# Kernel tuning notes

Hardware: AMD Instinct MI355X
Metric: run time of the kernel (lower is better)

The kernel has to match this reference:

```python
import jax, jax.numpy as jnp
import numpy as np

# Dims per init_kwargs
B, C_IN, H, W = 64, 512, 28, 28
GROWTH, BN_SIZE = 32, 4
C_MID = BN_SIZE * GROWTH  # 128
EPS = 1e-5
NUM_BITS = 8          # activation & weight quantization bits
NUM_CHUNKS = 16       # RangeBN chunking (eladhoffer quantize.py default)


def quantize(x, num_bits):
    """Uniform min/max quantize-dequantize (UniformQuantize forward)."""
    mn = x.min()
    mx = x.max()
    qmax = 2.0 ** num_bits - 1.0
    scale = jnp.maximum((mx - mn) / qmax, 1e-8)
    q = jnp.round((jnp.clip(x, mn, mx) - mn) / scale)
    return q * scale + mn


def conv2d(x, w, pad):
    return jax.lax.conv_general_dilated(
        x, w, window_strides=(1, 1), padding=[(pad, pad), (pad, pad)],
        dimension_numbers=('NCHW', 'OIHW', 'NCHW'))


def batchnorm2d(x, w, b):
    # training-mode BN: batch statistics over (N,H,W), biased variance
    mean = x.mean(axis=(0, 2, 3), keepdims=True)
    var = x.var(axis=(0, 2, 3), keepdims=True)
    xhat = (x - mean) * jax.lax.rsqrt(var + EPS)
    return xhat * w.reshape(1, -1, 1, 1) + b.reshape(1, -1, 1, 1)


def range_bn(x, w, b):
    # Range-based BN (training-mode): per-channel mean, scale from chunked min/max range
    Bx, Cx, Hx, Wx = x.shape
    y = x.transpose(1, 0, 2, 3).reshape(Cx, NUM_CHUNKS, -1)  # [C, chunks, n]
    mean_max = y.max(-1).mean(-1)   # [C]
    mean_min = y.min(-1).mean(-1)   # [C]
    mean = y.reshape(Cx, -1).mean(-1)  # [C]
    n = y.shape[-1]
    scale_fix = (0.5 * 0.35) * (1.0 + (np.pi * np.log(4.0)) ** 0.5) / ((2.0 * np.log(float(n))) ** 0.5)
    scale = 1.0 / ((mean_max - mean_min) * scale_fix + EPS)
    out = (x - mean.reshape(1, Cx, 1, 1)) * scale.reshape(1, Cx, 1, 1)
    qw = quantize(w, NUM_BITS)
    qb = quantize(b, NUM_BITS)
    return out * qw.reshape(1, Cx, 1, 1) + qb.reshape(1, Cx, 1, 1)


def setup_inputs() -> dict:
    key = jax.random.key(0)
    ks = jax.random.split(key, 7)
    x = jax.random.normal(ks[0], (B, C_IN, H, W), dtype=jnp.float32)
    bn1_w = jax.random.uniform(ks[1], (C_IN,), dtype=jnp.float32, minval=0.5, maxval=1.5)
    bn1_b = jax.random.normal(ks[2], (C_IN,), dtype=jnp.float32) * 0.1
    conv1_w = jax.random.normal(ks[3], (C_MID, C_IN, 1, 1), dtype=jnp.float32) * (2.0 / C_IN) ** 0.5
    rbn_w = jax.random.uniform(ks[4], (C_MID,), dtype=jnp.float32, minval=0.5, maxval=1.5)
    rbn_b = jax.random.normal(ks[5], (C_MID,), dtype=jnp.float32) * 0.1
    conv2_w = jax.random.normal(ks[6], (GROWTH, C_MID, 3, 3), dtype=jnp.float32) * (2.0 / (9 * C_MID)) ** 0.5
    return {"x": x, "bn1_w": bn1_w, "bn1_b": bn1_b, "conv1_w": conv1_w,
            "rbn_w": rbn_w, "rbn_b": rbn_b, "conv2_w": conv2_w}


def reference(x, bn1_w, bn1_b, conv1_w, rbn_w, rbn_b, conv2_w):
    # norm1 -> relu1 -> QConv2d(1x1) -> RangeBN -> relu2 -> QConv2d(3x3) -> concat
    h = jax.nn.relu(batchnorm2d(x, bn1_w, bn1_b))
    h = conv2d(quantize(h, NUM_BITS), quantize(conv1_w, NUM_BITS), pad=0)
    h = jax.nn.relu(range_bn(h, rbn_w, rbn_b))
    h = conv2d(quantize(h, NUM_BITS), quantize(conv2_w, NUM_BITS), pad=1)
    # drop_rate = 0 -> dropout is identity
    return jnp.concatenate([x, h], axis=1)
```

## Files before the change

### kernel.cpp

```cpp
#include <hip/hip_runtime.h>
#include <math.h>

static constexpr int BB    = 64;
static constexpr int C_IN  = 512;
static constexpr int C_MID = 128;
static constexpr int C_OUT = 32;
static constexpr int C_TOT = 544;
static constexpr int HW    = 784;

static constexpr size_t H2_OFF    = 0;
static constexpr size_t QW1_OFF   = 6422528;
static constexpr size_t QW2_OFF   = QW1_OFF + 65536;
static constexpr size_t PSTAT_OFF = QW2_OFF + 49152;
static constexpr size_t BNA_OFF   = PSTAT_OFF + 16384;
static constexpr size_t BNB_OFF   = BNA_OFF + 512;
static constexpr size_t CMAX_OFF  = BNB_OFF + 512;
static constexpr size_t CMIN_OFF  = CMAX_OFF + 2048;
static constexpr size_t CSUM_OFF  = CMIN_OFF + 2048;
static constexpr size_t A2_OFF    = CSUM_OFF + 2048;
static constexpr size_t B2_OFF    = A2_OFF + 128;
static constexpr size_t QRW_OFF   = B2_OFF + 128;
static constexpr size_t QRB_OFF   = QRW_OFF + 128;
static constexpr size_t SCAL_OFF  = QRB_OFF + 128;
static constexpr size_t PART_OFF  = SCAL_OFF + 16;
static constexpr size_t RP_OFF    = PART_OFF + 128;
static constexpr size_t PART2_OFF = RP_OFF + 172032;

#define DEVFN __device__ __forceinline__

typedef __bf16 bf16x8 __attribute__((ext_vector_type(8)));
typedef float  f32x4  __attribute__((ext_vector_type(4)));

DEVFN float qact(float v, float mn, float mx, float inv, float sc) {
    v = fminf(fmaxf(v, mn), mx);
    return fmaf(rintf((v - mn) * inv), sc, mn);
}

DEVFN unsigned f2bf(float f) {
    unsigned u = __float_as_uint(f);
    return (u + 0x7fffu + ((u >> 16) & 1u)) >> 16;
}

__global__ __launch_bounds__(256) void k_stats(const float* __restrict__ x,
                                               float* __restrict__ ws) {
    const int c = blockIdx.x, bg = blockIdx.y, tid = threadIdx.x;
    float s = 0.f, s2 = 0.f, mn = INFINITY, mx = -INFINITY;
    if (tid < 224) {
#pragma unroll
        for (int k = 0; k < 7; ++k) {
            const int idx = k * 224 + tid;
            const int b = bg * 8 + idx / 196, j = idx % 196;
            const float4 v = ((const float4*)(x + ((size_t)b * C_IN + c) * HW))[j];
            s  += (v.x + v.y) + (v.z + v.w);
            s2 += v.x * v.x + v.y * v.y + v.z * v.z + v.w * v.w;
            mn = fminf(mn, fminf(fminf(v.x, v.y), fminf(v.z, v.w)));
            mx = fmaxf(mx, fmaxf(fmaxf(v.x, v.y), fmaxf(v.z, v.w)));
        }
    }
    __shared__ float r0[256], r1[256], r2[256], r3[256];
    r0[tid] = s; r1[tid] = s2; r2[tid] = mn; r3[tid] = mx;
    __syncthreads();
    for (int off = 128; off > 0; off >>= 1) {
        if (tid < off) {
            r0[tid] += r0[tid + off];
            r1[tid] += r1[tid + off];
            r2[tid] = fminf(r2[tid], r2[tid + off]);
            r3[tid] = fmaxf(r3[tid], r3[tid + off]);
        }
        __syncthreads();
    }
    if (tid == 0) {
        float* p = ws + PSTAT_OFF + ((size_t)c * 8 + bg) * 4;
        p[0] = r0[0]; p[1] = r1[0]; p[2] = r2[0]; p[3] = r3[0];
    }
}

__global__ __launch_bounds__(256) void k_prep_red(const float* __restrict__ conv1_w,
                                                  const float* __restrict__ conv2_w,
                                                  const float* __restrict__ bn1_w,
                                                  const float* __restrict__ bn1_b,
                                                  float* __restrict__ ws) {
    const int b = blockIdx.x, tid = threadIdx.x;
    __shared__ float ra[256], rb[256];
    float mn = INFINITY, mx = -INFINITY;

    if (b < 32) {
        const float4* src = (const float4*)conv1_w + (size_t)b * 512;
        for (int i = tid; i < 512; i += 256) {
            const float4 v = src[i];
            mn = fminf(mn, fminf(fminf(v.x, v.y), fminf(v.z, v.w)));
            mx = fmaxf(mx, fmaxf(fmaxf(v.x, v.y), fmaxf(v.z, v.w)));
        }
    } else if (b < 40) {
        const float4* src = (const float4*)conv2_w + (size_t)(b - 32) * 1152;
        for (int i = tid; i < 1152; i += 256) {
            const float4 v = src[i];
            mn = fminf(mn, fminf(fminf(v.x, v.y), fminf(v.z, v.w)));
            mx = fmaxf(mx, fmaxf(fmaxf(v.x, v.y), fmaxf(v.z, v.w)));
        }
    } else {
        if (tid < 128) {
            const int c = (b - 40) * 128 + tid;
            const float* p = ws + PSTAT_OFF + (size_t)c * 32;
            float s = 0.f, s2 = 0.f, cmn = INFINITY, cmx = -INFINITY;
            for (int g = 0; g < 8; ++g) {
                s += p[g * 4 + 0]; s2 += p[g * 4 + 1];
                cmn = fminf(cmn, p[g * 4 + 2]); cmx = fmaxf(cmx, p[g * 4 + 3]);
            }
            const float n = 50176.f;
            const float mean = s / n;
            const float var  = s2 / n - mean * mean;
            const float rstd = rsqrtf(var + 1e-5f);
            const float A  = rstd * bn1_w[c];
            const float Bc = bn1_b[c] - mean * A;
            ws[BNA_OFF + c] = A; ws[BNB_OFF + c] = Bc;
            const float v1 = A * cmn + Bc, v2 = A * cmx + Bc;
            mn = fmaxf(0.f, fminf(v1, v2));
            mx = fmaxf(0.f, fmaxf(v1, v2));
        }
    }
    ra[tid] = mn; rb[tid] = mx;
    __syncthreads();
    for (int off = 128; off > 0; off >>= 1) {
        if (tid < off) { ra[tid] = fminf(ra[tid], ra[tid + off]); rb[tid] = fmaxf(rb[tid], rb[tid + off]); }
        __syncthreads();
    }
    if (tid == 0) {
        float* p;
        if (b < 32)       p = ws + PART_OFF + (size_t)b * 2;
        else if (b < 40)  p = ws + PART_OFF + 64 + (size_t)(b - 32) * 2;
        else              p = ws + PART_OFF + 80 + (size_t)(b - 40) * 2;
        p[0] = ra[0]; p[1] = rb[0];
    }
}

__global__ __launch_bounds__(256) void k_prep_fin(const float* __restrict__ rbn_w,
                                                  const float* __restrict__ rbn_b,
                                                  float* __restrict__ ws) {
    const int tid = threadIdx.x;
    __shared__ float ra[256], rb[256];
    __shared__ float s_mn, s_sc;

    ra[tid] = tid < 32 ? ws[PART_OFF + tid * 2] : INFINITY;
    rb[tid] = tid < 32 ? ws[PART_OFF + tid * 2 + 1] : -INFINITY;
    __syncthreads();
    for (int off = 128; off > 0; off >>= 1) {
        if (tid < off) { ra[tid] = fminf(ra[tid], ra[tid + off]); rb[tid] = fmaxf(rb[tid], rb[tid + off]); }
        __syncthreads();
    }
    if (tid == 0) {
        ws[SCAL_OFF + 8] = ra[0];
        ws[SCAL_OFF + 9] = fmaxf((rb[0] - ra[0]) / 255.f, 1e-8f);
    }
    __syncthreads();

    ra[tid] = tid < 8 ? ws[PART_OFF + 64 + tid * 2] : INFINITY;
    rb[tid] = tid < 8 ? ws[PART_OFF + 64 + tid * 2 + 1] : -INFINITY;
    __syncthreads();
    for (int off = 128; off > 0; off >>= 1) {
        if (tid < off) { ra[tid] = fminf(ra[tid], ra[tid + off]); rb[tid] = fmaxf(rb[tid], rb[tid + off]); }
        __syncthreads();
    }
    if (tid == 0) {
        ws[SCAL_OFF + 10] = ra[0];
        ws[SCAL_OFF + 11] = fmaxf((rb[0] - ra[0]) / 255.f, 1e-8f);
    }
    __syncthreads();

    ra[tid] = tid < 4 ? ws[PART_OFF + 80 + tid * 2] : INFINITY;
    rb[tid] = tid < 4 ? ws[PART_OFF + 80 + tid * 2 + 1] : -INFINITY;
    __syncthreads();
    for (int off = 128; off > 0; off >>= 1) {
        if (tid < off) { ra[tid] = fminf(ra[tid], ra[tid + off]); rb[tid] = fmaxf(rb[tid], rb[tid + off]); }
        __syncthreads();
    }
    if (tid == 0) {
        const float mn1 = ra[0], mx1 = rb[0];
        const float sc = fmaxf((mx1 - mn1) / 255.f, 1e-8f);
        ws[SCAL_OFF + 0] = mn1; ws[SCAL_OFF + 1] = sc; ws[SCAL_OFF + 2] = 1.f / sc; ws[SCAL_OFF + 6] = mx1;
    }
    __syncthreads();

    for (int which = 0; which < 2; ++which) {
        const float* src = which ? rbn_b : rbn_w;
        const size_t dst = which ? QRB_OFF : QRW_OFF;
        float v = 0.f;
        ra[tid] = INFINITY; rb[tid] = -INFINITY;
        if (tid < 128) { v = src[tid]; ra[tid] = v; rb[tid] = v; }
        __syncthreads();
        for (int off = 128; off > 0; off >>= 1) {
            if (tid < off) { ra[tid] = fminf(ra[tid], ra[tid + off]); rb[tid] = fmaxf(rb[tid], rb[tid + off]); }
            __syncthreads();
        }
        if (tid == 0) { s_mn = ra[0]; s_sc = fmaxf((rb[0] - ra[0]) / 255.f, 1e-8f); }
        __syncthreads();
        if (tid < 128) ws[dst + tid] = fmaf(rintf((v - s_mn) / s_sc), s_sc, s_mn);
        __syncthreads();
    }
}

__global__ __launch_bounds__(256) void k_prep_quant(const float* __restrict__ conv1_w,
                                                    const float* __restrict__ conv2_w,
                                                    float* __restrict__ ws) {
    const int b = blockIdx.x, tid = threadIdx.x;
    if (b < 32) {
        const float mnw = ws[SCAL_OFF + 8], scw = ws[SCAL_OFF + 9];
        unsigned short* qw = (unsigned short*)(ws + QW1_OFF);
        const int base = b * 2048;
#pragma unroll
        for (int t = 0; t < 8; ++t) {
            const int i = base + t * 256 + tid;
            const int co = i >> 9, k = i & 511;
            const float v = conv1_w[i];
            const float qv = fmaf(rintf((v - mnw) / scw), scw, mnw);
            const int ks = k >> 6, kc = (k >> 3) & 7, klo = k & 7;
            qw[(((size_t)ks * 128 + co) << 6) + (((kc ^ (co & 7)) << 3) | klo)] = (unsigned short)f2bf(qv);
        }
    } else {
        const float mnw = ws[SCAL_OFF + 10], scw = ws[SCAL_OFF + 11];
        unsigned short* qw2 = (unsigned short*)(ws + QW2_OFF);
        const int base = (b - 32) * 4608;
        for (int i2 = tid; i2 < 4608; i2 += 256) {
            const int i = base + i2;
            const int co = i / 1152, r = i % 1152, ci = r / 9, tap = r % 9;
            const float v = conv2_w[i];
            const float qv = fmaf(rintf((v - mnw) / scw), scw, mnw);
            qw2[(size_t)co * 1152 + tap * 128 + ci] = (unsigned short)f2bf(qv);
        }
    }
}

__global__ __launch_bounds__(256, 2) void k_conv1(const float* __restrict__ x,
                                                  float* __restrict__ out,
                                                  float* __restrict__ ws) {
    __shared__ __align__(16) unsigned short wt[128 * 64];
    __shared__ __align__(16) unsigned short ht[112 * 64];
    const int tid = threadIdx.x;
    const int pt = blockIdx.x, b = blockIdx.y;
    const int p0 = pt * 112;
    const float mn1 = ws[SCAL_OFF + 0], sc1 = ws[SCAL_OFF + 1];
    const float inv1 = ws[SCAL_OFF + 2], mx1 = ws[SCAL_OFF + 6];
    const unsigned short* qw1 = (const unsigned short*)(ws + QW1_OFF);
    const float* xb = x + (size_t)b * C_IN * HW;
    float* outb = out + (size_t)b * C_TOT * HW;

    const int o = tid & 7, q = tid >> 3;
    const int wv = tid >> 6, g = (tid >> 4) & 3, r4 = tid & 15;

    f32x4 acc[2][7];
#pragma unroll
    for (int i = 0; i < 2; ++i)
#pragma unroll
        for (int j = 0; j < 7; ++j) acc[i][j] = f32x4{0.f, 0.f, 0.f, 0.f};

    for (int ks = 0; ks < 8; ++ks) {
        const float4* wsrc = (const float4*)(qw1 + (size_t)ks * 8192);
        float4* wdst = (float4*)wt;
#pragma unroll
        for (int i = 0; i < 4; ++i) wdst[tid + i * 256] = wsrc[tid + i * 256];

        if (tid < 224) {
            const int ci0 = ks * 64 + o * 8;
            float vv[8][4];
#pragma unroll
            for (int j = 0; j < 8; ++j) {
                const f32x4 v = *(const f32x4*)(xb + (size_t)(ci0 + j) * HW + p0 + q * 4);
                __builtin_nontemporal_store(v, (f32x4*)(outb + (size_t)(ci0 + j) * HW + p0 + q * 4));
                const float A = ws[BNA_OFF + ci0 + j], Bc = ws[BNB_OFF + ci0 + j];
                vv[j][0] = qact(fmaxf(0.f, fmaf(v.x, A, Bc)), mn1, mx1, inv1, sc1);
                vv[j][1] = qact(fmaxf(0.f, fmaf(v.y, A, Bc)), mn1, mx1, inv1, sc1);
                vv[j][2] = qact(fmaxf(0.f, fmaf(v.z, A, Bc)), mn1, mx1, inv1, sc1);
                vv[j][3] = qact(fmaxf(0.f, fmaf(v.w, A, Bc)), mn1, mx1, inv1, sc1);
            }
#pragma unroll
            for (int r = 0; r < 4; ++r) {
                const int p = q * 4 + r;
                uint4 pk;
                pk.x = f2bf(vv[0][r]) | (f2bf(vv[1][r]) << 16);
                pk.y = f2bf(vv[2][r]) | (f2bf(vv[3][r]) << 16);
                pk.z = f2bf(vv[4][r]) | (f2bf(vv[5][r]) << 16);
                pk.w = f2bf(vv[6][r]) | (f2bf(vv[7][r]) << 16);
                *(uint4*)&ht[p * 64 + ((o ^ (p & 7)) << 3)] = pk;
            }
        }
        __syncthreads();

#pragma unroll
        for (int ksub = 0; ksub < 2; ++ksub) {
            const int kk = ksub * 4 + g;
            bf16x8 af[2], bfr[7];
#pragma unroll
            for (int ct = 0; ct < 2; ++ct) {
                const int co = wv * 32 + ct * 16 + r4;
                af[ct] = *(const bf16x8*)&wt[co * 64 + ((kk ^ (co & 7)) << 3)];
            }
#pragma unroll
            for (int pf = 0; pf < 7; ++pf) {
                const int p = pf * 16 + r4;
                bfr[pf] = *(const bf16x8*)&ht[p * 64 + ((kk ^ (p & 7)) << 3)];
            }
#pragma unroll
            for (int ct = 0; ct < 2; ++ct)
#pragma unroll
                for (int pf = 0; pf < 7; ++pf)
                    acc[ct][pf] = __builtin_amdgcn_mfma_f32_16x16x32_bf16(af[ct], bfr[pf], acc[ct][pf], 0, 0, 0);
        }
        __syncthreads();
    }

    float* hb = ws + H2_OFF + (size_t)b * C_MID * HW;
#pragma unroll
    for (int ct = 0; ct < 2; ++ct) {
        const int co0 = wv * 32 + ct * 16 + g * 4;
#pragma unroll
        for (int pf = 0; pf < 7; ++pf) {
            const int p = p0 + pf * 16 + r4;
#pragma unroll
            for (int r = 0; r < 4; ++r)
                hb[(size_t)(co0 + r) * HW + p] = acc[ct][pf][r];
        }
    }

#pragma unroll
    for (int ct = 0; ct < 2; ++ct)
#pragma unroll
        for (int r = 0; r < 4; ++r) {
            float s = 0.f, mn = INFINITY, mx = -INFINITY;
#pragma unroll
            for (int pf = 0; pf < 7; ++pf) {
                const float v = acc[ct][pf][r];
                s += v; mn = fminf(mn, v); mx = fmaxf(mx, v);
            }
#pragma unroll
            for (int m = 1; m < 16; m <<= 1) {
                s  += __shfl_xor(s, m, 64);
                mn  = fminf(mn, __shfl_xor(mn, m, 64));
                mx  = fmaxf(mx, __shfl_xor(mx, m, 64));
            }
            if (r4 == 0) {
                const int co = wv * 32 + ct * 16 + g * 4 + r;
                float* dst = ws + RP_OFF + (((size_t)co * 64 + b) * 7 + pt) * 3;
                dst[0] = s; dst[1] = mn; dst[2] = mx;
            }
        }
}

__global__ __launch_bounds__(64) void k_rbn_combine(float* __restrict__ ws) {
    const int c = blockIdx.x, t = threadIdx.x;
    const int ch = t >> 2, sub = t & 3;
    const int b = ch * 4 + sub;
    const float* rp = ws + RP_OFF + ((size_t)c * 64 + b) * 21;
    float s = 0.f, mn = INFINITY, mx = -INFINITY;
#pragma unroll
    for (int pt = 0; pt < 7; ++pt) {
        s += rp[pt * 3 + 0];
        mn = fminf(mn, rp[pt * 3 + 1]);
        mx = fmaxf(mx, rp[pt * 3 + 2]);
    }
#pragma unroll
    for (int m = 1; m < 4; m <<= 1) {
        s  += __shfl_xor(s, m, 64);
        mn  = fminf(mn, __shfl_xor(mn, m, 64));
        mx  = fmaxf(mx, __shfl_xor(mx, m, 64));
    }
    float smx = mx, smn = mn, stot = s, gmn = mn, gmx = mx;
#pragma unroll
    for (int m = 4; m < 64; m <<= 1) {
        smx  += __shfl_xor(smx, m, 64);
        smn  += __shfl_xor(smn, m, 64);
        stot += __shfl_xor(stot, m, 64);
        gmn   = fminf(gmn, __shfl_xor(gmn, m, 64));
        gmx   = fmaxf(gmx, __shfl_xor(gmx, m, 64));
    }
    if (t == 0) {
        const float mm = smx * (1.f / 16.f), mnm = smn * (1.f / 16.f);
        const float mean = stot / 50176.f;
        const double PI_D = 3.14159265358979323846;
        const double sfd = 0.175 * (1.0 + sqrt(PI_D * log(4.0))) / sqrt(2.0 * log(3136.0));
        const float scale = 1.f / ((mm - mnm) * (float)sfd + 1e-5f);
        const float A  = scale * ws[QRW_OFF + c];
        const float Bc = ws[QRB_OFF + c] - mean * A;
        ws[A2_OFF + c] = A; ws[B2_OFF + c] = Bc;
        const float v1 = A * gmn + Bc, v2 = A * gmx + Bc;
        ws[PART2_OFF + c * 2 + 0] = fmaxf(0.f, fminf(v1, v2));
        ws[PART2_OFF + c * 2 + 1] = fmaxf(0.f, fmaxf(v1, v2));
    }
}

__global__ __launch_bounds__(64) void k_prep2b(float* __restrict__ ws) {
    const int t = threadIdx.x;
    float lo = fminf(ws[PART2_OFF + t * 2], ws[PART2_OFF + (t + 64) * 2]);
    float hi = fmaxf(ws[PART2_OFF + t * 2 + 1], ws[PART2_OFF + (t + 64) * 2 + 1]);
#pragma unroll
    for (int m = 1; m < 64; m <<= 1) {
        lo = fminf(lo, __shfl_xor(lo, m, 64));
        hi = fmaxf(hi, __shfl_xor(hi, m, 64));
    }
    if (t == 0) {
        const float sc = fmaxf((hi - lo) / 255.f, 1e-8f);
        ws[SCAL_OFF + 3] = lo; ws[SCAL_OFF + 4] = sc; ws[SCAL_OFF + 5] = 1.f / sc; ws[SCAL_OFF + 7] = hi;
    }
}

__global__ __launch_bounds__(128) void k_conv2(float* __restrict__ out, const float* __restrict__ ws) {
    __shared__ __align__(16) unsigned short lact[7 * 30 * 128];
    const int tid = threadIdx.x;
    const int pt = blockIdx.x, b = blockIdx.y;
    const int y0 = pt * 4;
    const float mn3 = ws[SCAL_OFF + 3], sc3 = ws[SCAL_OFF + 4];
    const float inv3 = ws[SCAL_OFF + 5], mx3 = ws[SCAL_OFF + 7];

    {
        const uint4 z = {0u, 0u, 0u, 0u};
        uint4* lp = (uint4*)lact;
        for (int i = tid; i < 3360; i += 128) lp[i] = z;
    }
    __syncthreads();

    const float* h2b = ws + H2_OFF + (size_t)b * C_MID * HW;
    for (int task = tid; task < 672; task += 128) {
        const int oct = task / 42, rem = task % 42, r = rem / 7, xq = rem % 7;
        const int gy = y0 - 1 + r;
        if (gy < 0 || gy > 27) continue;
        float vv[8][4];
#pragma unroll
        for (int j = 0; j < 8; ++j) {
            const int ci = oct * 8 + j;
            const float4 v = *(const float4*)(h2b + (size_t)ci * HW + gy * 28 + xq * 4);
            const float A = ws[A2_OFF + ci], Bc = ws[B2_OFF + ci];
            vv[j][0] = qact(fmaxf(0.f, fmaf(v.x, A, Bc)), mn3, mx3, inv3, sc3);
            vv[j][1] = qact(fmaxf(0.f, fmaf(v.y, A, Bc)), mn3, mx3, inv3, sc3);
            vv[j][2] = qact(fmaxf(0.f, fmaf(v.z, A, Bc)), mn3, mx3, inv3, sc3);
            vv[j][3] = qact(fmaxf(0.f, fmaf(v.w, A, Bc)), mn3, mx3, inv3, sc3);
        }
#pragma unroll
        for (int xi = 0; xi < 4; ++xi) {
            const int col = xq * 4 + xi + 1;
            const int phys = (oct + col) & 15;
            uint4 pk;
            pk.x = f2bf(vv[0][xi]) | (f2bf(vv[1][xi]) << 16);
            pk.y = f2bf(vv[2][xi]) | (f2bf(vv[3][xi]) << 16);
            pk.z = f2bf(vv[4][xi]) | (f2bf(vv[5][xi]) << 16);
            pk.w = f2bf(vv[6][xi]) | (f2bf(vv[7][xi]) << 16);
            *(uint4*)&lact[((r * 30 + col) * 16 + phys) * 8] = pk;
        }
    }
    __syncthreads();

    const int wv = tid >> 6, lane = tid & 63, r4 = lane & 15, g = lane >> 4;
    int py[4], px[4];
#pragma unroll
    for (int i = 0; i < 4; ++i) {
        const int p = (wv * 4 + i) * 16 + r4;
        py[i] = p / 28; px[i] = p % 28;
    }
    f32x4 acc[2][4];
#pragma unroll
    for (int ct = 0; ct < 2; ++ct)
#pragma unroll
        for (int i = 0; i < 4; ++i) acc[ct][i] = f32x4{0.f, 0.f, 0.f, 0.f};

    const unsigned short* qw2 = (const unsigned short*)(ws + QW2_OFF);
    for (int tap = 0; tap < 9; ++tap) {
        const int dy = tap / 3, dx = tap % 3;
        bf16x8 afr[2][4];
#pragma unroll
        for (int ct = 0; ct < 2; ++ct)
#pragma unroll
            for (int c4 = 0; c4 < 4; ++c4) {
                const int co = ct * 16 + r4;
                afr[ct][c4] = *(const bf16x8*)&qw2[(size_t)co * 1152 + tap * 128 + c4 * 32 + g * 8];
            }
#pragma unroll
        for (int c4 = 0; c4 < 4; ++c4) {
            bf16x8 bfr[4];
#pragma unroll
            for (int i = 0; i < 4; ++i) {
                const int row = py[i] + dy, col = px[i] + dx;
                const int phys = (c4 * 4 + g + col) & 15;
                bfr[i] = *(const bf16x8*)&lact[((row * 30 + col) * 16 + phys) * 8];
            }
#pragma unroll
            for (int ct = 0; ct < 2; ++ct)
#pragma unroll
                for (int i = 0; i < 4; ++i)
                    acc[ct][i] = __builtin_amdgcn_mfma_f32_16x16x32_bf16(afr[ct][c4], bfr[i], acc[ct][i], 0, 0, 0);
        }
    }

#pragma unroll
    for (int ct = 0; ct < 2; ++ct)
#pragma unroll
        for (int i = 0; i < 4; ++i) {
            const int pf = wv * 4 + i;
            if (pf < 7) {
                const int p = pf * 16 + r4;
#pragma unroll
                for (int r = 0; r < 4; ++r) {
                    const int co = ct * 16 + g * 4 + r;
                    out[((size_t)b * C_TOT + 512 + co) * HW + y0 * 28 + p] = acc[ct][i][r];
                }
            }
        }
}

extern "C" void kernel_launch(void* const* d_in, const int* in_sizes, int n_in,
                              void* d_out, int out_size, void* d_ws, size_t ws_size,
                              hipStream_t stream) {
    const float* x       = (const float*)d_in[0];
    const float* bn1_w   = (const float*)d_in[1];
    const float* bn1_b   = (const float*)d_in[2];
    const float* conv1_w = (const float*)d_in[3];
    const float* rbn_w   = (const float*)d_in[4];
    const float* rbn_b   = (const float*)d_in[5];
    const float* conv2_w = (const float*)d_in[6];
    float* out = (float*)d_out;
    float* ws  = (float*)d_ws;

    k_stats<<<dim3(512, 8), 256, 0, stream>>>(x, ws);
    k_prep_red<<<44, 256, 0, stream>>>(conv1_w, conv2_w, bn1_w, bn1_b, ws);
    k_prep_fin<<<1, 256, 0, stream>>>(rbn_w, rbn_b, ws);
    k_prep_quant<<<40, 256, 0, stream>>>(conv1_w, conv2_w, ws);
    k_conv1<<<dim3(7, 64), 256, 0, stream>>>(x, out, ws);
    k_rbn_combine<<<128, 64, 0, stream>>>(ws);
    k_prep2b<<<1, 64, 0, stream>>>(ws);
    k_conv2<<<dim3(7, 64), 128, 0, stream>>>(out, ws);
}
```

Before: 106.1 us.

## Merge prep kernels using atomic min/max cells to cut launch count

Weight min/max reductions move into the stats kernel as extra blocks that publish results through atomic min/max on order-preserving integer keys. The separate prep reduce, finalize and quantize kernels are merged into one prep kernel. The final activation range is found with atomics in the combine kernel, and conv2 derives its scale itself. This replaces four small serial launches with two (plus a tiny init kernel), reducing launch and serialization overhead. It adds atomic contention and relies on the unsigned bit order of non-negative floats for the second range.

```diff
diff --git a/kernel.cpp b/kernel.cpp
--- a/kernel.cpp
+++ b/kernel.cpp
@@ -14,17 +14,13 @@
 static constexpr size_t PSTAT_OFF = QW2_OFF + 49152;
 static constexpr size_t BNA_OFF   = PSTAT_OFF + 16384;
 static constexpr size_t BNB_OFF   = BNA_OFF + 512;
-static constexpr size_t CMAX_OFF  = BNB_OFF + 512;
-static constexpr size_t CMIN_OFF  = CMAX_OFF + 2048;
-static constexpr size_t CSUM_OFF  = CMIN_OFF + 2048;
-static constexpr size_t A2_OFF    = CSUM_OFF + 2048;
+static constexpr size_t A2_OFF    = BNB_OFF + 512;
 static constexpr size_t B2_OFF    = A2_OFF + 128;
 static constexpr size_t QRW_OFF   = B2_OFF + 128;
 static constexpr size_t QRB_OFF   = QRW_OFF + 128;
 static constexpr size_t SCAL_OFF  = QRB_OFF + 128;
-static constexpr size_t PART_OFF  = SCAL_OFF + 16;
-static constexpr size_t RP_OFF    = PART_OFF + 128;
-static constexpr size_t PART2_OFF = RP_OFF + 172032;
+static constexpr size_t ACELL_OFF = SCAL_OFF + 16;
+static constexpr size_t RP_OFF    = ACELL_OFF + 112;
 
 #define DEVFN __device__ __forceinline__
 
@@ -41,66 +37,132 @@
     return (u + 0x7fffu + ((u >> 16) & 1u)) >> 16;
 }
 
+DEVFN unsigned fkey(float f) {
+    const unsigned u = __float_as_uint(f);
+    return (u & 0x80000000u) ? ~u : (u | 0x80000000u);
+}
+DEVFN float funkey(unsigned k) {
+    const unsigned u = (k & 0x80000000u) ? (k & 0x7FFFFFFFu) : ~k;
+    return __uint_as_float(u);
+}
+
+__global__ void k_init(float* __restrict__ ws) {
+    unsigned* cells = (unsigned*)(ws + ACELL_OFF);
+    const int t = threadIdx.x;
+    if (t < 3) cells[t] = 0xFFFFFFFFu;
+    else if (t < 6) cells[4 + (t - 3)] = 0u;
+}
+
 __global__ __launch_bounds__(256) void k_stats(const float* __restrict__ x,
+                                               const float* __restrict__ conv1_w,
+                                               const float* __restrict__ conv2_w,
                                                float* __restrict__ ws) {
-    const int c = blockIdx.x, bg = blockIdx.y, tid = threadIdx.x;
-    float s = 0.f, s2 = 0.f, mn = INFINITY, mx = -INFINITY;
-    if (tid < 224) {
-#pragma unroll
-        for (int k = 0; k < 7; ++k) {
-            const int idx = k * 224 + tid;
-            const int b = bg * 8 + idx / 196, j = idx % 196;
-            const float4 v = ((const float4*)(x + ((size_t)b * C_IN + c) * HW))[j];
-            s  += (v.x + v.y) + (v.z + v.w);
-            s2 += v.x * v.x + v.y * v.y + v.z * v.z + v.w * v.w;
-            mn = fminf(mn, fminf(fminf(v.x, v.y), fminf(v.z, v.w)));
-            mx = fmaxf(mx, fmaxf(fmaxf(v.x, v.y), fmaxf(v.z, v.w)));
-        }
-    }
+    const int bid = blockIdx.x, tid = threadIdx.x;
     __shared__ float r0[256], r1[256], r2[256], r3[256];
-    r0[tid] = s; r1[tid] = s2; r2[tid] = mn; r3[tid] = mx;
-    __syncthreads();
-    for (int off = 128; off > 0; off >>= 1) {
-        if (tid < off) {
-            r0[tid] += r0[tid + off];
-            r1[tid] += r1[tid + off];
-            r2[tid] = fminf(r2[tid], r2[tid + off]);
-            r3[tid] = fmaxf(r3[tid], r3[tid + off]);
-        }
+
+    if (bid < 4096) {
+        const int c = bid >> 3, bg = bid & 7;
+        float s = 0.f, s2 = 0.f, mn = INFINITY, mx = -INFINITY;
+        if (tid < 224) {
+#pragma unroll
+            for (int k = 0; k < 7; ++k) {
+                const int idx = k * 224 + tid;
+                const int b = bg * 8 + idx / 196, j = idx % 196;
+                const float4 v = ((const float4*)(x + ((size_t)b * C_IN + c) * HW))[j];
+                s  += (v.x + v.y) + (v.z + v.w);
+                s2 += v.x * v.x + v.y * v.y + v.z * v.z + v.w * v.w;
+                mn = fminf(mn, fminf(fminf(v.x, v.y), fminf(v.z, v.w)));
+                mx = fmaxf(mx, fmaxf(fmaxf(v.x, v.y), fmaxf(v.z, v.w)));
+            }
+        }
+        r0[tid] = s; r1[tid] = s2; r2[tid] = mn; r3[tid] = mx;
         __syncthreads();
-    }
-    if (tid == 0) {
-        float* p = ws + PSTAT_OFF + ((size_t)c * 8 + bg) * 4;
-        p[0] = r0[0]; p[1] = r1[0]; p[2] = r2[0]; p[3] = r3[0];
-    }
-}
-
-__global__ __launch_bounds__(256) void k_prep_red(const float* __restrict__ conv1_w,
-                                                  const float* __restrict__ conv2_w,
-                                                  const float* __restrict__ bn1_w,
-                                                  const float* __restrict__ bn1_b,
-                                                  float* __restrict__ ws) {
+        for (int off = 128; off > 0; off >>= 1) {
+            if (tid < off) {
+                r0[tid] += r0[tid + off];
+                r1[tid] += r1[tid + off];
+                r2[tid] = fminf(r2[tid], r2[tid + off]);
+                r3[tid] = fmaxf(r3[tid], r3[tid + off]);
+            }
+            __syncthreads();
+        }
+        if (tid == 0) {
+            float* p = ws + PSTAT_OFF + ((size_t)c * 8 + bg) * 4;
+            p[0] = r0[0]; p[1] = r1[0]; p[2] = r2[0]; p[3] = r3[0];
+        }
+    } else {
+        float mn = INFINITY, mx = -INFINITY;
+        if (bid < 4128) {
+            const float4* src = (const float4*)conv1_w + (size_t)(bid - 4096) * 512;
+            for (int i = tid; i < 512; i += 256) {
+                const float4 v = src[i];
+                mn = fminf(mn, fminf(fminf(v.x, v.y), fminf(v.z, v.w)));
+                mx = fmaxf(mx, fmaxf(fmaxf(v.x, v.y), fmaxf(v.z, v.w)));
+            }
+        } else {
+            const float4* src = (const float4*)conv2_w + (size_t)(bid - 4128) * 1152;
+            for (int i = tid; i < 1152; i += 256) {
+                const float4 v = src[i];
+                mn = fminf(mn, fminf(fminf(v.x, v.y), fminf(v.z, v.w)));
+                mx = fmaxf(mx, fmaxf(fmaxf(v.x, v.y), fmaxf(v.z, v.w)));
+            }
+        }
+        r2[tid] = mn; r3[tid] = mx;
+        __syncthreads();
+        for (int off = 128; off > 0; off >>= 1) {
+            if (tid < off) { r2[tid] = fminf(r2[tid], r2[tid + off]); r3[tid] = fmaxf(r3[tid], r3[tid + off]); }
+            __syncthreads();
+        }
+        if (tid == 0) {
+            unsigned* cells = (unsigned*)(ws + ACELL_OFF);
+            const int w = (bid < 4128) ? 0 : 1;
+            atomicMin(&cells[w],     fkey(r2[0]));
+            atomicMax(&cells[4 + w], fkey(r3[0]));
+        }
+    }
+}
+
+__global__ __launch_bounds__(256) void k_prep(const float* __restrict__ conv1_w,
+                                              const float* __restrict__ conv2_w,
+                                              const float* __restrict__ bn1_w,
+                                              const float* __restrict__ bn1_b,
+                                              const float* __restrict__ rbn_w,
+                                              const float* __restrict__ rbn_b,
+                                              float* __restrict__ ws) {
     const int b = blockIdx.x, tid = threadIdx.x;
+    const unsigned* cells = (const unsigned*)(ws + ACELL_OFF);
     __shared__ float ra[256], rb[256];
-    float mn = INFINITY, mx = -INFINITY;
+    __shared__ float s_mn, s_sc;
 
     if (b < 32) {
-        const float4* src = (const float4*)conv1_w + (size_t)b * 512;
-        for (int i = tid; i < 512; i += 256) {
-            const float4 v = src[i];
-            mn = fminf(mn, fminf(fminf(v.x, v.y), fminf(v.z, v.w)));
-            mx = fmaxf(mx, fmaxf(fmaxf(v.x, v.y), fmaxf(v.z, v.w)));
+        const float mnw = funkey(cells[0]), mxw = funkey(cells[4]);
+        const float scw = fmaxf((mxw - mnw) / 255.f, 1e-8f);
+        unsigned short* qw = (unsigned short*)(ws + QW1_OFF);
+        const int base = b * 2048;
+#pragma unroll
+        for (int t = 0; t < 8; ++t) {
+            const int i = base + t * 256 + tid;
+            const int co = i >> 9, k = i & 511;
+            const float v = conv1_w[i];
+            const float qv = fmaf(rintf((v - mnw) / scw), scw, mnw);
+            const int ks = k >> 6, kc = (k >> 3) & 7, klo = k & 7;
+            qw[(((size_t)ks * 128 + co) << 6) + (((kc ^ (co & 7)) << 3) | klo)] = (unsigned short)f2bf(qv);
         }
     } else if (b < 40) {
-        const float4* src = (const float4*)conv2_w + (size_t)(b - 32) * 1152;
-        for (int i = tid; i < 1152; i += 256) {
-            const float4 v = src[i];
-            mn = fminf(mn, fminf(fminf(v.x, v.y), fminf(v.z, v.w)));
-            mx = fmaxf(mx, fmaxf(fmaxf(v.x, v.y), fmaxf(v.z, v.w)));
-        }
-    } else {
-        if (tid < 128) {
-            const int c = (b - 40) * 128 + tid;
+        const float mnw = funkey(cells[1]), mxw = funkey(cells[5]);
+        const float scw = fmaxf((mxw - mnw) / 255.f, 1e-8f);
+        unsigned short* qw2 = (unsigned short*)(ws + QW2_OFF);
+        const int base = (b - 32) * 4608;
+        for (int i2 = tid; i2 < 4608; i2 += 256) {
+            const int i = base + i2;
+            const int co = i / 1152, r = i % 1152, ci = r / 9, tap = r % 9;
+            const float v = conv2_w[i];
+            const float qv = fmaf(rintf((v - mnw) / scw), scw, mnw);
+            qw2[(size_t)co * 1152 + tap * 128 + ci] = (unsigned short)f2bf(qv);
+        }
+    } else if (b == 40) {
+        float lmn = INFINITY, lmx = -INFINITY;
+        for (int c = tid; c < 512; c += 256) {
             const float* p = ws + PSTAT_OFF + (size_t)c * 32;
             float s = 0.f, s2 = 0.f, cmn = INFINITY, cmx = -INFINITY;
             for (int g = 0; g < 8; ++g) {
@@ -115,117 +177,36 @@
             const float Bc = bn1_b[c] - mean * A;
             ws[BNA_OFF + c] = A; ws[BNB_OFF + c] = Bc;
             const float v1 = A * cmn + Bc, v2 = A * cmx + Bc;
-            mn = fmaxf(0.f, fminf(v1, v2));
-            mx = fmaxf(0.f, fmaxf(v1, v2));
-        }
-    }
-    ra[tid] = mn; rb[tid] = mx;
-    __syncthreads();
-    for (int off = 128; off > 0; off >>= 1) {
-        if (tid < off) { ra[tid] = fminf(ra[tid], ra[tid + off]); rb[tid] = fmaxf(rb[tid], rb[tid + off]); }
-        __syncthreads();
-    }
-    if (tid == 0) {
-        float* p;
-        if (b < 32)       p = ws + PART_OFF + (size_t)b * 2;
-        else if (b < 40)  p = ws + PART_OFF + 64 + (size_t)(b - 32) * 2;
-        else              p = ws + PART_OFF + 80 + (size_t)(b - 40) * 2;
-        p[0] = ra[0]; p[1] = rb[0];
-    }
-}
-
-__global__ __launch_bounds__(256) void k_prep_fin(const float* __restrict__ rbn_w,
-                                                  const float* __restrict__ rbn_b,
-                                                  float* __restrict__ ws) {
-    const int tid = threadIdx.x;
-    __shared__ float ra[256], rb[256];
-    __shared__ float s_mn, s_sc;
-
-    ra[tid] = tid < 32 ? ws[PART_OFF + tid * 2] : INFINITY;
-    rb[tid] = tid < 32 ? ws[PART_OFF + tid * 2 + 1] : -INFINITY;
-    __syncthreads();
-    for (int off = 128; off > 0; off >>= 1) {
-        if (tid < off) { ra[tid] = fminf(ra[tid], ra[tid + off]); rb[tid] = fmaxf(rb[tid], rb[tid + off]); }
-        __syncthreads();
-    }
-    if (tid == 0) {
-        ws[SCAL_OFF + 8] = ra[0];
-        ws[SCAL_OFF + 9] = fmaxf((rb[0] - ra[0]) / 255.f, 1e-8f);
-    }
-    __syncthreads();
-
-    ra[tid] = tid < 8 ? ws[PART_OFF + 64 + tid * 2] : INFINITY;
-    rb[tid] = tid < 8 ? ws[PART_OFF + 64 + tid * 2 + 1] : -INFINITY;
-    __syncthreads();
-    for (int off = 128; off > 0; off >>= 1) {
-        if (tid < off) { ra[tid] = fminf(ra[tid], ra[tid + off]); rb[tid] = fmaxf(rb[tid], rb[tid + off]); }
-        __syncthreads();
-    }
-    if (tid == 0) {
-        ws[SCAL_OFF + 10] = ra[0];
-        ws[SCAL_OFF + 11] = fmaxf((rb[0] - ra[0]) / 255.f, 1e-8f);
-    }
-    __syncthreads();
-
-    ra[tid] = tid < 4 ? ws[PART_OFF + 80 + tid * 2] : INFINITY;
-    rb[tid] = tid < 4 ? ws[PART_OFF + 80 + tid * 2 + 1] : -INFINITY;
-    __syncthreads();
-    for (int off = 128; off > 0; off >>= 1) {
-        if (tid < off) { ra[tid] = fminf(ra[tid], ra[tid + off]); rb[tid] = fmaxf(rb[tid], rb[tid + off]); }
-        __syncthreads();
-    }
-    if (tid == 0) {
-        const float mn1 = ra[0], mx1 = rb[0];
-        const float sc = fmaxf((mx1 - mn1) / 255.f, 1e-8f);
-        ws[SCAL_OFF + 0] = mn1; ws[SCAL_OFF + 1] = sc; ws[SCAL_OFF + 2] = 1.f / sc; ws[SCAL_OFF + 6] = mx1;
-    }
-    __syncthreads();
-
-    for (int which = 0; which < 2; ++which) {
-        const float* src = which ? rbn_b : rbn_w;
-        const size_t dst = which ? QRB_OFF : QRW_OFF;
-        float v = 0.f;
-        ra[tid] = INFINITY; rb[tid] = -INFINITY;
-        if (tid < 128) { v = src[tid]; ra[tid] = v; rb[tid] = v; }
+            lmn = fminf(lmn, fmaxf(0.f, fminf(v1, v2)));
+            lmx = fmaxf(lmx, fmaxf(0.f, fmaxf(v1, v2)));
+        }
+        ra[tid] = lmn; rb[tid] = lmx;
         __syncthreads();
         for (int off = 128; off > 0; off >>= 1) {
             if (tid < off) { ra[tid] = fminf(ra[tid], ra[tid + off]); rb[tid] = fmaxf(rb[tid], rb[tid + off]); }
             __syncthreads();
         }
-        if (tid == 0) { s_mn = ra[0]; s_sc = fmaxf((rb[0] - ra[0]) / 255.f, 1e-8f); }
-        __syncthreads();
-        if (tid < 128) ws[dst + tid] = fmaf(rintf((v - s_mn) / s_sc), s_sc, s_mn);
-        __syncthreads();
-    }
-}
-
-__global__ __launch_bounds__(256) void k_prep_quant(const float* __restrict__ conv1_w,
-                                                    const float* __restrict__ conv2_w,
-                                                    float* __restrict__ ws) {
-    const int b = blockIdx.x, tid = threadIdx.x;
-    if (b < 32) {
-        const float mnw = ws[SCAL_OFF + 8], scw = ws[SCAL_OFF + 9];
-        unsigned short* qw = (unsigned short*)(ws + QW1_OFF);
-        const int base = b * 2048;
-#pragma unroll
-        for (int t = 0; t < 8; ++t) {
-            const int i = base + t * 256 + tid;
-            const int co = i >> 9, k = i & 511;
-            const float v = conv1_w[i];
-            const float qv = fmaf(rintf((v - mnw) / scw), scw, mnw);
-            const int ks = k >> 6, kc = (k >> 3) & 7, klo = k & 7;
-            qw[(((size_t)ks * 128 + co) << 6) + (((kc ^ (co & 7)) << 3) | klo)] = (unsigned short)f2bf(qv);
+        if (tid == 0) {
+            const float mn1 = ra[0], mx1 = rb[0];
+            const float sc = fmaxf((mx1 - mn1) / 255.f, 1e-8f);
+            ws[SCAL_OFF + 0] = mn1; ws[SCAL_OFF + 1] = sc; ws[SCAL_OFF + 2] = 1.f / sc; ws[SCAL_OFF + 6] = mx1;
         }
     } else {
-        const float mnw = ws[SCAL_OFF + 10], scw = ws[SCAL_OFF + 11];
-        unsigned short* qw2 = (unsigned short*)(ws + QW2_OFF);
-        const int base = (b - 32) * 4608;
-        for (int i2 = tid; i2 < 4608; i2 += 256) {
-            const int i = base + i2;
-            const int co = i / 1152, r = i % 1152, ci = r / 9, tap = r % 9;
-            const float v = conv2_w[i];
-            const float qv = fmaf(rintf((v - mnw) / scw), scw, mnw);
-            qw2[(size_t)co * 1152 + tap * 128 + ci] = (unsigned short)f2bf(qv);
+        for (int which = 0; which < 2; ++which) {
+            const float* src = which ? rbn_b : rbn_w;
+            const size_t dst = which ? QRB_OFF : QRW_OFF;
+            float v = 0.f;
+            ra[tid] = INFINITY; rb[tid] = -INFINITY;
+            if (tid < 128) { v = src[tid]; ra[tid] = v; rb[tid] = v; }
+            __syncthreads();
+            for (int off = 128; off > 0; off >>= 1) {
+                if (tid < off) { ra[tid] = fminf(ra[tid], ra[tid + off]); rb[tid] = fmaxf(rb[tid], rb[tid + off]); }
+                __syncthreads();
+            }
+            if (tid == 0) { s_mn = ra[0]; s_sc = fmaxf((rb[0] - ra[0]) / 255.f, 1e-8f); }
+            __syncthreads();
+            if (tid < 128) ws[dst + tid] = fmaf(rintf((v - s_mn) / s_sc), s_sc, s_mn);
+            __syncthreads();
         }
     }
 }
@@ -382,23 +363,11 @@
         const float Bc = ws[QRB_OFF + c] - mean * A;
         ws[A2_OFF + c] = A; ws[B2_OFF + c] = Bc;
         const float v1 = A * gmn + Bc, v2 = A * gmx + Bc;
-        ws[PART2_OFF + c * 2 + 0] = fmaxf(0.f, fminf(v1, v2));
-        ws[PART2_OFF + c * 2 + 1] = fmaxf(0.f, fmaxf(v1, v2));
-    }
-}
-
-__global__ __launch_bounds__(64) void k_prep2b(float* __restrict__ ws) {
-    const int t = threadIdx.x;
-    float lo = fminf(ws[PART2_OFF + t * 2], ws[PART2_OFF + (t + 64) * 2]);
-    float hi = fmaxf(ws[PART2_OFF + t * 2 + 1], ws[PART2_OFF + (t + 64) * 2 + 1]);
-#pragma unroll
-    for (int m = 1; m < 64; m <<= 1) {
-        lo = fminf(lo, __shfl_xor(lo, m, 64));
-        hi = fmaxf(hi, __shfl_xor(hi, m, 64));
-    }
-    if (t == 0) {
-        const float sc = fmaxf((hi - lo) / 255.f, 1e-8f);
-        ws[SCAL_OFF + 3] = lo; ws[SCAL_OFF + 4] = sc; ws[SCAL_OFF + 5] = 1.f / sc; ws[SCAL_OFF + 7] = hi;
+        const float lo = fmaxf(0.f, fminf(v1, v2));
+        const float hi = fmaxf(0.f, fmaxf(v1, v2));
+        unsigned* cells = (unsigned*)(ws + ACELL_OFF);
+        atomicMin(&cells[2], __float_as_uint(lo));
+        atomicMax(&cells[6], __float_as_uint(hi));
     }
 }
 
@@ -407,8 +376,11 @@
     const int tid = threadIdx.x;
     const int pt = blockIdx.x, b = blockIdx.y;
     const int y0 = pt * 4;
-    const float mn3 = ws[SCAL_OFF + 3], sc3 = ws[SCAL_OFF + 4];
-    const float inv3 = ws[SCAL_OFF + 5], mx3 = ws[SCAL_OFF + 7];
+    const unsigned* cells = (const unsigned*)(ws + ACELL_OFF);
+    const float mn3 = __uint_as_float(cells[2]);
+    const float mx3 = __uint_as_float(cells[6]);
+    const float sc3 = fmaxf((mx3 - mn3) / 255.f, 1e-8f);
+    const float inv3 = 1.f / sc3;
 
     {
         const uint4 z = {0u, 0u, 0u, 0u};
@@ -517,12 +489,10 @@
     float* out = (float*)d_out;
     float* ws  = (float*)d_ws;
 
-    k_stats<<<dim3(512, 8), 256, 0, stream>>>(x, ws);
-    k_prep_red<<<44, 256, 0, stream>>>(conv1_w, conv2_w, bn1_w, bn1_b, ws);
-    k_prep_fin<<<1, 256, 0, stream>>>(rbn_w, rbn_b, ws);
-    k_prep_quant<<<40, 256, 0, stream>>>(conv1_w, conv2_w, ws);
+    k_init<<<1, 64, 0, stream>>>(ws);
+    k_stats<<<4136, 256, 0, stream>>>(x, conv1_w, conv2_w, ws);
+    k_prep<<<42, 256, 0, stream>>>(conv1_w, conv2_w, bn1_w, bn1_b, rbn_w, rbn_b, ws);
     k_conv1<<<dim3(7, 64), 256, 0, stream>>>(x, out, ws);
     k_rbn_combine<<<128, 64, 0, stream>>>(ws);
-    k_prep2b<<<1, 64, 0, stream>>>(ws);
     k_conv2<<<dim3(7, 64), 128, 0, stream>>>(out, ws);
 }
```

New measurement: 102.2 us. 1.04x faster.
